# Performance work log

Hardware: AMD Instinct MI355X
Metric: run time of the kernel (lower is better)

## Reference

```python
import jax, jax.numpy as jnp
import numpy as np

L, B, T, N, M = 2, 32, 256, 1024, 1024  # layers, batch, time, input feat, hidden


def setup_inputs() -> dict:
    key = jax.random.key(0)
    ks = jax.random.split(key, 7)
    s = 0.02  # weight init scale
    return {
        "x": jax.random.normal(ks[0], (B, T, N), dtype=jnp.float32),
        "h": jax.random.normal(ks[1], (L, B, M), dtype=jnp.float32) * 0.1,
        "c": jax.random.normal(ks[2], (L, B, M), dtype=jnp.float32) * 0.1,
        "Wih": jax.random.normal(ks[3], (L, 4 * M, N), dtype=jnp.float32) * s,
        "Whh": jax.random.normal(ks[4], (L, 4 * M, M), dtype=jnp.float32) * s,
        "bih": jnp.zeros((L, 4 * M), dtype=jnp.float32),
        "bhh": jnp.zeros((L, 4 * M), dtype=jnp.float32),
    }


def _lstm_cell(x_t, h_t, c_t, Wih_l, Whh_l, b_l):
    # gates: [i | f | g | o], matching torch.nn.LSTMCell layout
    gates = x_t @ Wih_l.T + h_t @ Whh_l.T + b_l  # (B, 4M)
    i, f, g, o = jnp.split(gates, 4, axis=-1)
    i, f, o = jax.nn.sigmoid(i), jax.nn.sigmoid(f), jax.nn.sigmoid(o)
    c_new = f * c_t + i * jnp.tanh(g)
    h_new = o * jnp.tanh(c_new)
    return h_new, c_new


def reference(x, h, c, Wih, Whh, bih, bhh):
    b_sum = bih + bhh  # (L, 4M)

    def step(carry, x_t):
        h_cur, c_cur = carry  # each (L, B, M)
        hs, cs = [], []
        inp = x_t
        for l in range(L):  # small fixed layer loop
            h_l, c_l = _lstm_cell(inp, h_cur[l], c_cur[l], Wih[l], Whh[l], b_sum[l])
            hs.append(h_l)
            cs.append(c_l)
            inp = h_l
        return (jnp.stack(hs, 0), jnp.stack(cs, 0)), inp  # emit top-layer h

    (h_final, c_final), outs_tbm = jax.lax.scan(step, (h, c), jnp.swapaxes(x, 0, 1))
    outs = jnp.swapaxes(outs_tbm, 0, 1)  # (B, T, M)
    return outs, h_final, c_final
```

## Files before the change

kernel.cpp:

```cpp
#include <hip/hip_runtime.h>


typedef __bf16 bf16x8 __attribute__((ext_vector_type(8)));
typedef float  f32x4  __attribute__((ext_vector_type(4)));
typedef unsigned u32x4 __attribute__((ext_vector_type(4)));

__device__ __forceinline__ unsigned short f2bf(float f) {
    union { float f; unsigned u; } v; v.f = f;
    unsigned u = v.u;
    unsigned r = u + 0x7fffu + ((u >> 16) & 1u);
    return (unsigned short)(r >> 16);
}
__device__ __forceinline__ float sigmoidf_fast(float x) {
    return 1.0f / (1.0f + __expf(-x));
}
__device__ __forceinline__ float tanhf_fast(float x) {
    return 1.0f - 2.0f / (__expf(2.0f * x) + 1.0f);
}

__global__ void cvt_w_concat(const float* __restrict__ src,
                             unsigned short* __restrict__ dst, int off, int n4) {
    int i = blockIdx.x * blockDim.x + threadIdx.x;
    int stride = gridDim.x * blockDim.x;
    for (; i < n4; i += stride) {
        float4 v = ((const float4*)src)[i];
        ushort4 o;
        o.x = f2bf(v.x); o.y = f2bf(v.y); o.z = f2bf(v.z); o.w = f2bf(v.w);
        int row = i >> 8;
        int c4  = i & 255;
        *(ushort4*)&dst[(size_t)row * 2048 + off + c4 * 4] = o;
    }
}

__global__ void cvt_x_tiles(const float* __restrict__ x,
                            unsigned short* __restrict__ xT) {
    int t = blockIdx.x, tid = threadIdx.x;
    unsigned short* tile = xT + (size_t)t * 32768;
    for (int b = 0; b < 32; ++b) {
        float4 v = *(const float4*)&x[((size_t)b * 256 + t) * 1024 + tid * 4];
        ushort4 o;
        o.x = f2bf(v.x); o.y = f2bf(v.y); o.z = f2bf(v.z); o.w = f2bf(v.w);
        *(ushort4*)&tile[(tid >> 2) * 512 + b * 16 + (tid & 3) * 4] = o;
    }
}

__global__ void cvt_h0_tiles(const float* __restrict__ h0,
                             unsigned short* __restrict__ h0T) {
    int l = blockIdx.x, tid = threadIdx.x;
    unsigned short* tile = h0T + (size_t)l * 32768;
    for (int b = 0; b < 32; ++b) {
        float4 v = *(const float4*)&h0[((size_t)l * 32 + b) * 1024 + tid * 4];
        ushort4 o;
        o.x = f2bf(v.x); o.y = f2bf(v.y); o.z = f2bf(v.z); o.w = f2bf(v.w);
        *(ushort4*)&tile[(tid >> 2) * 512 + b * 16 + (tid & 3) * 4] = o;
    }
}

__global__ void out_transpose(const float* __restrict__ outT,
                              float* __restrict__ out) {
    int t = blockIdx.x, tid = threadIdx.x;
    const float* tile = outT + (size_t)t * 32768;
    for (int b = 0; b < 32; ++b) {
        float4 v = *(const float4*)&tile[(tid >> 2) * 512 + b * 16 + (tid & 3) * 4];
        *(float4*)&out[((size_t)b * 256 + t) * 1024 + tid * 4] = v;
    }
}

__device__ __forceinline__ void pollge(const unsigned* fp, unsigned tgt) {
    while (true) {
        unsigned v = __hip_atomic_load(fp, __ATOMIC_RELAXED,
                                       __HIP_MEMORY_SCOPE_AGENT);
        if (__all((int)(v >= tgt))) break;
        __builtin_amdgcn_s_sleep(1);
    }
}

__global__ __launch_bounds__(256, 1) void lstm_fused(
    const unsigned short* __restrict__ Wcat,
    const unsigned short* __restrict__ xT,
    unsigned short* __restrict__ seqT,
    const unsigned short* __restrict__ h0T,
    unsigned short* __restrict__ hparT,
    float* __restrict__ outT,
    const float* __restrict__ c0,
    const float* __restrict__ bih, const float* __restrict__ bhh,
    float* __restrict__ out, unsigned int* flags)
{
    __shared__ __align__(16) unsigned short buf[32][1024];
    __shared__ __align__(16) float gred[4][2][4][16][20];
    __shared__ __align__(16) unsigned short hout_bf[32][16];
    __shared__ __align__(16) float hout_f[32][16];

    const int tid  = threadIdx.x;
    const int lane = tid & 63;
    const int w    = tid >> 6;
    const int l    = blockIdx.x >> 6;
    const int bidl = blockIdx.x & 63;
    const int m0   = bidl * 16;
    const int n    = lane & 15;
    const int g    = lane >> 4;
    const int lk   = g * 8;
    const int nn7  = n & 7;

    bf16x8 wx[32], wh[32];
    const unsigned short* Wl = Wcat + (size_t)l * 4096 * 2048;
    #pragma unroll
    for (int ct = 0; ct < 4; ct++) {
        int vc = ct * 16 + n;
        size_t jrow = (size_t)((vc & 3) * 1024 + m0 + (vc >> 2));
        #pragma unroll
        for (int kc = 0; kc < 8; kc++) {
            wx[ct*8+kc] = *(const bf16x8*)&Wl[jrow*2048 +        w*256 + kc*32 + lk];
            wh[ct*8+kc] = *(const bf16x8*)&Wl[jrow*2048 + 1024 + w*256 + kc*32 + lk];
        }
    }

    const int eb = lane >> 1;
    const int q  = lane & 1;
    const int em = m0 + 4 * w + 2 * q;
    float bs0[4], bs1[4];
    #pragma unroll
    for (int gg = 0; gg < 4; gg++) {
        bs0[gg] = bih[l*4096 + gg*1024 + em]     + bhh[l*4096 + gg*1024 + em];
        bs1[gg] = bih[l*4096 + gg*1024 + em + 1] + bhh[l*4096 + gg*1024 + em + 1];
    }
    float2 creg = *(const float2*)&c0[(size_t)l * 32768 + eb * 1024 + em];
    float2 hlast = {0.f, 0.f};
    const int uh = eb >> 4, urow = eb & 15;

    char* const bufb = (char*)&buf[0][0];
    const int sb     = lane >> 1;
    const int halfk  = lane & 1;
    const int srcOff = w * 16384 + sb * 32 + halfk * 16;
    const int sbRow  = sb * 2048;
    const int ldsCol = w * 512 + halfk * 16;
    const int swz    = (sb & 7) << 4;

    const int hb64 = (nn7 >> 2) * 64;
    const int gx16 = (g ^ (nn7 & 3)) * 16;
    const int rOffA0 = n * 2048 + w * 512 + gx16 + hb64;
    const int rOffA1 = n * 2048 + w * 512 + gx16 + (64 - hb64);

    f32x4 acc0[4] = {}, acc1[4] = {};

    auto stage_gemm = [&](const char* tb, const bf16x8* wfv, bool byp) {
        u32x4 hv[16];
        const char* gp = tb + srcOff;
        if (byp) {
            #pragma unroll
            for (int si = 0; si < 16; si++)
                asm volatile("global_load_dwordx4 %0, %1, off sc0 sc1"
                             : "=v"(hv[si]) : "v"(gp + si * 1024) : "memory");
        } else {
            #pragma unroll
            for (int si = 0; si < 16; si++)
                asm volatile("global_load_dwordx4 %0, %1, off"
                             : "=v"(hv[si]) : "v"(gp + si * 1024) : "memory");
        }
        const char* pA0 = bufb + rOffA0;
        const char* pA1 = bufb + rOffA1;
        const char* pB0 = pA0 + 16 * 2048;
        const char* pB1 = pA1 + 16 * 2048;
#define SGRP(G4, VM) \
        asm volatile("s_waitcnt vmcnt(" VM ")" ::: "memory"); \
        _Pragma("unroll") \
        for (int si = 4*(G4); si < 4*(G4)+4; si++) \
            *(u32x4*)(bufb + sbRow + ((ldsCol + si*32) ^ swz)) = hv[si]; \
        { \
            bf16x8 a0 = *(const bf16x8*)(pA0 + (G4)*128); \
            bf16x8 a1 = *(const bf16x8*)(pB0 + (G4)*128); \
            _Pragma("unroll") \
            for (int ct = 0; ct < 4; ct++) { \
                acc0[ct] = __builtin_amdgcn_mfma_f32_16x16x32_bf16(a0, wfv[ct*8+2*(G4)],   acc0[ct],0,0,0); \
                acc1[ct] = __builtin_amdgcn_mfma_f32_16x16x32_bf16(a1, wfv[ct*8+2*(G4)],   acc1[ct],0,0,0); \
            } \
            bf16x8 b0 = *(const bf16x8*)(pA1 + (G4)*128); \
            bf16x8 b1 = *(const bf16x8*)(pB1 + (G4)*128); \
            _Pragma("unroll") \
            for (int ct = 0; ct < 4; ct++) { \
                acc0[ct] = __builtin_amdgcn_mfma_f32_16x16x32_bf16(b0, wfv[ct*8+2*(G4)+1], acc0[ct],0,0,0); \
                acc1[ct] = __builtin_amdgcn_mfma_f32_16x16x32_bf16(b1, wfv[ct*8+2*(G4)+1], acc1[ct],0,0,0); \
            } \
        }
        SGRP(0, "12") SGRP(1, "8") SGRP(2, "4") SGRP(3, "0")
#undef SGRP
    };

    if (l == 0) stage_gemm((const char*)xT, wx, false);

    const int lag = l * 2;
    #pragma unroll 1
    for (int s = 0; s < 258; s++) {
        const int  t   = s - lag;
        const bool act = (t >= 0) && (t < 256);

        if (act) {
            const char* hb = (t == 0)
                ? (const char*)(h0T + (size_t)l * 32768)
                : (l == 0 ? (const char*)(seqT + (size_t)(t - 1) * 32768)
                          : (const char*)(hparT + (size_t)((t - 1) & 1) * 32768));
            stage_gemm(hb, wh, true);

            {
                int r0 = g * 4;
                #pragma unroll
                for (int ct = 0; ct < 4; ct++) {
                    *(f32x4*)&gred[w][0][ct][n][r0] = acc0[ct];
                    *(f32x4*)&gred[w][1][ct][n][r0] = acc1[ct];
                }
            }
            __syncthreads();
            float g8[8];
            #pragma unroll
            for (int j = 0; j < 8; j++) {
                g8[j] = (gred[0][uh][w][8*q+j][urow] + gred[1][uh][w][8*q+j][urow])
                      + (gred[2][uh][w][8*q+j][urow] + gred[3][uh][w][8*q+j][urow]);
            }
            float gi0 = g8[0] + bs0[0], gf0 = g8[1] + bs0[1];
            float gg0 = g8[2] + bs0[2], go0 = g8[3] + bs0[3];
            float gi1 = g8[4] + bs1[0], gf1 = g8[5] + bs1[1];
            float gg1 = g8[6] + bs1[2], go1 = g8[7] + bs1[3];

            float c0n = sigmoidf_fast(gf0) * creg.x + sigmoidf_fast(gi0) * tanhf_fast(gg0);
            float c1n = sigmoidf_fast(gf1) * creg.y + sigmoidf_fast(gi1) * tanhf_fast(gg1);
            float h0v = sigmoidf_fast(go0) * tanhf_fast(c0n);
            float h1v = sigmoidf_fast(go1) * tanhf_fast(c1n);
            creg.x = c0n; creg.y = c1n;
            hlast.x = h0v; hlast.y = h1v;

            unsigned hp = (unsigned)f2bf(h0v) | ((unsigned)f2bf(h1v) << 16);
            *(unsigned*)&hout_bf[eb][4*w + 2*q] = hp;
            if (l == 1) {
                float2 hv2 = {h0v, h1v};
                *(float2*)&hout_f[eb][4*w + 2*q] = hv2;
            }
            __syncthreads();
            if (tid < 64) {
                u32x4 v = *(const u32x4*)((const char*)&hout_bf[0][0] + tid * 16);
                const char* dp = (l == 0)
                    ? (const char*)(seqT  + (size_t)t * 32768)       + bidl * 1024 + tid * 16
                    : (const char*)(hparT + (size_t)(t & 1) * 32768) + bidl * 1024 + tid * 16;
                asm volatile("global_store_dwordx4 %0, %1, off sc0 sc1"
                             :: "v"(dp), "v"(v) : "memory");
                asm volatile("s_waitcnt vmcnt(0)" ::: "memory");
                if (tid == 0)
                    __hip_atomic_store(flags + l * 64 + bidl, (unsigned)(s + 1),
                                       __ATOMIC_RELAXED, __HIP_MEMORY_SCOPE_AGENT);
            } else if (l == 1 && tid < 192) {
                int u = tid - 64;
                f32x4 v = *(const f32x4*)((const char*)&hout_f[0][0] + u * 16);
                *(f32x4*)((char*)outT + (size_t)t * 131072 + bidl * 2048 + u * 16) = v;
            }
        } else if (tid == 0) {
            __hip_atomic_store(flags + l * 64 + bidl, (unsigned)(s + 1),
                               __ATOMIC_RELAXED, __HIP_MEMORY_SCOPE_AGENT);
        }

        const int  tn   = t + 1;
        const bool xact = (tn >= ((l == 0) ? 1 : 0)) && (tn <= 255);
        if (xact) {
            #pragma unroll
            for (int ct = 0; ct < 4; ct++) {
                acc0[ct] = (f32x4){0.f, 0.f, 0.f, 0.f};
                acc1[ct] = (f32x4){0.f, 0.f, 0.f, 0.f};
            }
            stage_gemm(l == 0 ? (const char*)(xT   + (size_t)tn * 32768)
                              : (const char*)(seqT + (size_t)tn * 32768),
                       wx, l == 1);
        }

        if (tid < 128) pollge(flags + tid, (unsigned)(s + 1));
        __syncthreads();
    }

    float* hF = out + (size_t)8192 * 1024 + (size_t)l * 32768;
    float* cF = out + (size_t)8192 * 1024 + 65536 + (size_t)l * 32768;
    float2 hf2 = {hlast.x, hlast.y};
    *(float2*)&hF[eb * 1024 + em] = hf2;
    float2 cf2 = {creg.x, creg.y};
    *(float2*)&cF[eb * 1024 + em] = cf2;
}

extern "C" void kernel_launch(void* const* d_in, const int* in_sizes, int n_in,
                              void* d_out, int out_size, void* d_ws, size_t ws_size,
                              hipStream_t stream)
{
    const float* x   = (const float*)d_in[0];
    const float* h0  = (const float*)d_in[1];
    const float* c0  = (const float*)d_in[2];
    const float* Wih = (const float*)d_in[3];
    const float* Whh = (const float*)d_in[4];
    const float* bih = (const float*)d_in[5];
    const float* bhh = (const float*)d_in[6];
    float* out = (float*)d_out;

    char* p = (char*)d_ws;
    unsigned short* xT    = (unsigned short*)p; p += (size_t)256 * 32768 * 2;
    unsigned short* seqT  = (unsigned short*)p; p += (size_t)256 * 32768 * 2;
    unsigned short* Wcat  = (unsigned short*)p; p += (size_t)2 * 4096 * 2048 * 2;
    unsigned short* h0T   = (unsigned short*)p; p += (size_t)2 * 32768 * 2;
    unsigned short* hparT = (unsigned short*)p; p += (size_t)2 * 32768 * 2;
    float*          outT  = (float*)p;          p += (size_t)256 * 32768 * 4;
    unsigned int*   flags = (unsigned int*)p;   p += 4096;

    hipMemsetAsync(flags, 0, 4096, stream);
    cvt_w_concat<<<1024, 256, 0, stream>>>(Wih, Wcat, 0,    2 * 4096 * 256);
    cvt_w_concat<<<1024, 256, 0, stream>>>(Whh, Wcat, 1024, 2 * 4096 * 256);
    cvt_x_tiles<<<256, 256, 0, stream>>>(x, xT);
    cvt_h0_tiles<<<2, 256, 0, stream>>>(h0, h0T);

    lstm_fused<<<128, 256, 0, stream>>>(Wcat, xT, seqT, h0T, hparT, outT,
                                        c0, bih, bhh, out, flags);

    out_transpose<<<256, 256, 0, stream>>>(outT, out);
}
```

Measured before the change: 1.321 ms.

## Prefetch next-step input tile during LSTM epilogue and relax layer-0 polling

Splits the shared staging buffer into separate hidden-state and input buffers. The gate-reduction scratch is aliased onto the input buffer to save LDS. Global loads for the next timestep's input tile are now issued right after the recurrent GEMM, so their latency overlaps the gate epilogue and h store; wave 0 issues its loads after it finishes storing h. Layer-0 blocks now poll only layer-0 flags instead of both layers, which removes a cross-layer sync dependency. The cost is tighter register pressure from keeping the prefetched tile live across the epilogue, and correctness now depends on the aliased scratch being free when the input tile is written.

Measured after the change: 1.526 ms. +15.5%, slower.

```diff
diff --git a/kernel.cpp b/kernel.cpp
--- a/kernel.cpp
+++ b/kernel.cpp
@@ -86,8 +86,8 @@
     const float* __restrict__ bih, const float* __restrict__ bhh,
     float* __restrict__ out, unsigned int* flags)
 {
-    __shared__ __align__(16) unsigned short buf[32][1024];
-    __shared__ __align__(16) float gred[4][2][4][16][20];
+    __shared__ __align__(16) unsigned short bufH[32][1024];
+    __shared__ __align__(16) unsigned short bufX[32][1024];
     __shared__ __align__(16) unsigned short hout_bf[32][16];
     __shared__ __align__(16) float hout_f[32][16];
 
@@ -102,6 +102,10 @@
     const int lk   = g * 8;
     const int nn7  = n & 7;
 
+    char* const bH = (char*)&bufH[0][0];
+    char* const bX = (char*)&bufX[0][0];
+    float (*gred)[2][4][16][20] = (float (*)[2][4][16][20])bX;
+
     bf16x8 wx[32], wh[32];
     const unsigned short* Wl = Wcat + (size_t)l * 4096 * 2048;
     #pragma unroll
@@ -128,7 +132,6 @@
     float2 hlast = {0.f, 0.f};
     const int uh = eb >> 4, urow = eb & 15;
 
-    char* const bufb = (char*)&buf[0][0];
     const int sb     = lane >> 1;
     const int halfk  = lane & 1;
     const int srcOff = w * 16384 + sb * 32 + halfk * 16;
@@ -142,9 +145,9 @@
     const int rOffA1 = n * 2048 + w * 512 + gx16 + (64 - hb64);
 
     f32x4 acc0[4] = {}, acc1[4] = {};
-
-    auto stage_gemm = [&](const char* tb, const bf16x8* wfv, bool byp) {
-        u32x4 hv[16];
+    u32x4 hv[16];
+
+    auto issue = [&](const char* tb, bool byp) {
         const char* gp = tb + srcOff;
         if (byp) {
             #pragma unroll
@@ -157,49 +160,95 @@
                 asm volatile("global_load_dwordx4 %0, %1, off"
                              : "=v"(hv[si]) : "v"(gp + si * 1024) : "memory");
         }
-        const char* pA0 = bufb + rOffA0;
-        const char* pA1 = bufb + rOffA1;
+    };
+
+    auto gemmbuf = [&](const char* base, const bf16x8* wfv) {
+        const char* pA0 = base + rOffA0;
+        const char* pA1 = base + rOffA1;
+        const char* pB0 = pA0 + 16 * 2048;
+        const char* pB1 = pA1 + 16 * 2048;
+        #pragma unroll
+        for (int kc2 = 0; kc2 < 4; kc2++) {
+            bf16x8 a0 = *(const bf16x8*)(pA0 + kc2 * 128);
+            bf16x8 a1 = *(const bf16x8*)(pB0 + kc2 * 128);
+            #pragma unroll
+            for (int ct = 0; ct < 4; ct++) {
+                acc0[ct] = __builtin_amdgcn_mfma_f32_16x16x32_bf16(a0, wfv[ct*8+2*kc2],   acc0[ct],0,0,0);
+                acc1[ct] = __builtin_amdgcn_mfma_f32_16x16x32_bf16(a1, wfv[ct*8+2*kc2],   acc1[ct],0,0,0);
+            }
+            bf16x8 b0 = *(const bf16x8*)(pA1 + kc2 * 128);
+            bf16x8 b1 = *(const bf16x8*)(pB1 + kc2 * 128);
+            #pragma unroll
+            for (int ct = 0; ct < 4; ct++) {
+                acc0[ct] = __builtin_amdgcn_mfma_f32_16x16x32_bf16(b0, wfv[ct*8+2*kc2+1], acc0[ct],0,0,0);
+                acc1[ct] = __builtin_amdgcn_mfma_f32_16x16x32_bf16(b1, wfv[ct*8+2*kc2+1], acc1[ct],0,0,0);
+            }
+        }
+    };
+
+    auto stage_gemm_h = [&](const char* tb) {
+        const char* gp = tb + srcOff;
+        #pragma unroll
+        for (int si = 0; si < 16; si++)
+            asm volatile("global_load_dwordx4 %0, %1, off sc0 sc1"
+                         : "=v"(hv[si]) : "v"(gp + si * 1024) : "memory");
+        const char* pA0 = bH + rOffA0;
+        const char* pA1 = bH + rOffA1;
         const char* pB0 = pA0 + 16 * 2048;
         const char* pB1 = pA1 + 16 * 2048;
 #define SGRP(G4, VM) \
         asm volatile("s_waitcnt vmcnt(" VM ")" ::: "memory"); \
         _Pragma("unroll") \
         for (int si = 4*(G4); si < 4*(G4)+4; si++) \
-            *(u32x4*)(bufb + sbRow + ((ldsCol + si*32) ^ swz)) = hv[si]; \
+            *(u32x4*)(bH + sbRow + ((ldsCol + si*32) ^ swz)) = hv[si]; \
         { \
             bf16x8 a0 = *(const bf16x8*)(pA0 + (G4)*128); \
             bf16x8 a1 = *(const bf16x8*)(pB0 + (G4)*128); \
             _Pragma("unroll") \
             for (int ct = 0; ct < 4; ct++) { \
-                acc0[ct] = __builtin_amdgcn_mfma_f32_16x16x32_bf16(a0, wfv[ct*8+2*(G4)],   acc0[ct],0,0,0); \
-                acc1[ct] = __builtin_amdgcn_mfma_f32_16x16x32_bf16(a1, wfv[ct*8+2*(G4)],   acc1[ct],0,0,0); \
+                acc0[ct] = __builtin_amdgcn_mfma_f32_16x16x32_bf16(a0, wh[ct*8+2*(G4)],   acc0[ct],0,0,0); \
+                acc1[ct] = __builtin_amdgcn_mfma_f32_16x16x32_bf16(a1, wh[ct*8+2*(G4)],   acc1[ct],0,0,0); \
             } \
             bf16x8 b0 = *(const bf16x8*)(pA1 + (G4)*128); \
             bf16x8 b1 = *(const bf16x8*)(pB1 + (G4)*128); \
             _Pragma("unroll") \
             for (int ct = 0; ct < 4; ct++) { \
-                acc0[ct] = __builtin_amdgcn_mfma_f32_16x16x32_bf16(b0, wfv[ct*8+2*(G4)+1], acc0[ct],0,0,0); \
-                acc1[ct] = __builtin_amdgcn_mfma_f32_16x16x32_bf16(b1, wfv[ct*8+2*(G4)+1], acc1[ct],0,0,0); \
+                acc0[ct] = __builtin_amdgcn_mfma_f32_16x16x32_bf16(b0, wh[ct*8+2*(G4)+1], acc0[ct],0,0,0); \
+                acc1[ct] = __builtin_amdgcn_mfma_f32_16x16x32_bf16(b1, wh[ct*8+2*(G4)+1], acc1[ct],0,0,0); \
             } \
         }
         SGRP(0, "12") SGRP(1, "8") SGRP(2, "4") SGRP(3, "0")
 #undef SGRP
     };
 
-    if (l == 0) stage_gemm((const char*)xT, wx, false);
+    if (l == 0) {
+        issue((const char*)xT, false);
+        asm volatile("s_waitcnt vmcnt(0)" ::: "memory");
+        #pragma unroll
+        for (int si = 0; si < 16; si++)
+            *(u32x4*)(bX + sbRow + ((ldsCol + si * 32) ^ swz)) = hv[si];
+        gemmbuf(bX, wx);
+    }
+    __syncthreads();
 
     const int lag = l * 2;
     #pragma unroll 1
     for (int s = 0; s < 258; s++) {
-        const int  t   = s - lag;
-        const bool act = (t >= 0) && (t < 256);
+        const int  t    = s - lag;
+        const bool act  = (t >= 0) && (t < 256);
+        const int  tn   = t + 1;
+        const bool xact = (tn >= ((l == 0) ? 1 : 0)) && (tn <= 255);
+        const char* xsrc = (l == 0) ? (const char*)(xT   + (size_t)tn * 32768)
+                                    : (const char*)(seqT + (size_t)tn * 32768);
 
         if (act) {
             const char* hb = (t == 0)
                 ? (const char*)(h0T + (size_t)l * 32768)
                 : (l == 0 ? (const char*)(seqT + (size_t)(t - 1) * 32768)
                           : (const char*)(hparT + (size_t)((t - 1) & 1) * 32768));
-            stage_gemm(hb, wh, true);
+            stage_gemm_h(hb);
+
+            if (xact && w != 0) issue(xsrc, l == 1);
 
             {
                 int r0 = g * 4;
@@ -251,25 +300,28 @@
                 f32x4 v = *(const f32x4*)((const char*)&hout_f[0][0] + u * 16);
                 *(f32x4*)((char*)outT + (size_t)t * 131072 + bidl * 2048 + u * 16) = v;
             }
-        } else if (tid == 0) {
-            __hip_atomic_store(flags + l * 64 + bidl, (unsigned)(s + 1),
-                               __ATOMIC_RELAXED, __HIP_MEMORY_SCOPE_AGENT);
-        }
-
-        const int  tn   = t + 1;
-        const bool xact = (tn >= ((l == 0) ? 1 : 0)) && (tn <= 255);
+            if (xact && w == 0) issue(xsrc, l == 1);
+        } else {
+            if (tid == 0)
+                __hip_atomic_store(flags + l * 64 + bidl, (unsigned)(s + 1),
+                                   __ATOMIC_RELAXED, __HIP_MEMORY_SCOPE_AGENT);
+            if (xact) issue(xsrc, l == 1);
+        }
+
         if (xact) {
+            asm volatile("s_waitcnt vmcnt(0)" ::: "memory");
+            #pragma unroll
+            for (int si = 0; si < 16; si++)
+                *(u32x4*)(bX + sbRow + ((ldsCol + si * 32) ^ swz)) = hv[si];
             #pragma unroll
             for (int ct = 0; ct < 4; ct++) {
                 acc0[ct] = (f32x4){0.f, 0.f, 0.f, 0.f};
                 acc1[ct] = (f32x4){0.f, 0.f, 0.f, 0.f};
             }
-            stage_gemm(l == 0 ? (const char*)(xT   + (size_t)tn * 32768)
-                              : (const char*)(seqT + (size_t)tn * 32768),
-                       wx, l == 1);
-        }
-
-        if (tid < 128) pollge(flags + tid, (unsigned)(s + 1));
+            gemmbuf(bX, wx);
+        }
+
+        if (tid < (l ? 128 : 64)) pollge(flags + tid, (unsigned)(s + 1));
         __syncthreads();
     }
 
```
